# Optimization experiments

Hardware: AMD Instinct MI355X
Metric: run time of the kernel (lower is better)

## Reference

```python
import jax, jax.numpy as jnp
import numpy as np

DT = 0.05
TAU = 10.0
V_TH = 2.0
ALPHA = 1.0 - DT / TAU  # membrane leak factor (1 - dt/tau)


def setup_inputs() -> dict:
    key = jax.random.key(0)
    kx, kw = jax.random.split(key)
    B, T, N = 32, 1024, 2048
    x = jax.random.normal(kx, (B, T, N), dtype=jnp.float32)
    # w ~ Normal(0, 1/sqrt(N)) as in torch.nn.init.normal_(std=1/sqrt(N))
    w = jax.random.normal(kw, (N,), dtype=jnp.float32) * float(1.0 / np.sqrt(N))
    return {"x": x, "w": w}


def reference(x, w):
    """LIF recurrence with online eligibility-trace gradient, fused over time.

    Per step t (matching NeuronClass.__call__ then backward_online):
      v   = alpha*v + x_t @ w - v_th * z          (z from previous step, detached)
      z   = 1[v > v_th]
      eps = x_t - v * w                            # [B, N]
      g  += v * eps + (eps @ w) * p                # p is the PRE-update trace
      p   = alpha*p + x_t
    Returns (v_seq [B,T], z_seq [B,T], grad_acc [B,N]).
    """
    B, T, N = x.shape
    alpha = jnp.asarray(ALPHA, x.dtype)
    v_th = jnp.asarray(V_TH, x.dtype)
    xt = jnp.swapaxes(x, 0, 1)  # [T, B, N] for scan over time

    def step(carry, x_t):
        v, z, p, g = carry
        v = alpha * v + x_t @ w - v_th * z          # [B]
        z = (v > v_th).astype(x_t.dtype)            # hard threshold
        eps = x_t - v[:, None] * w                  # [B, N] prediction error
        g = g + v[:, None] * eps + (eps @ w)[:, None] * p
        p = alpha * p + x_t                         # trace updated AFTER use
        return (v, z, p, g), (v, z)

    v0 = jnp.zeros((B,), x.dtype)
    z0 = jnp.zeros((B,), x.dtype)
    p0 = jnp.zeros((B, N), x.dtype)
    g0 = jnp.zeros((B, N), x.dtype)
    (_, _, _, grad_acc), (v_seq, z_seq) = jax.lax.scan(step, (v0, z0, p0, g0), xt)
    return jnp.swapaxes(v_seq, 0, 1), jnp.swapaxes(z_seq, 0, 1), grad_acc
```

## Files before the change

kernel.cpp:

```cpp
#include <hip/hip_runtime.h>


#define ALPHA 0.995f
#define VTH   2.0f

constexpr int B = 32;
constexpr int T = 1024;
constexpr int N = 2048;
constexpr int CT = 128;
constexpr int NCH = T / CT;
constexpr int TCH = 64;
constexpr int NTC = T / TCH;

__global__ __launch_bounds__(256) void gemv_kernel(const float* __restrict__ x,
                                                   const float* __restrict__ w,
                                                   float* __restrict__ uT) {
    const int wave = threadIdx.x >> 6;
    const int lane = threadIdx.x & 63;
    const int row0 = blockIdx.x * 8 + wave * 2;
    const float* xr0 = x + (size_t)row0 * N;
    const float* xr1 = xr0 + N;
    float s0 = 0.f, s1 = 0.f;
#pragma unroll
    for (int k = 0; k < 8; ++k) {
        const int idx = k * 256 + lane * 4;
        const float4 wv = *reinterpret_cast<const float4*>(w + idx);
        const float4 a  = *reinterpret_cast<const float4*>(xr0 + idx);
        const float4 b  = *reinterpret_cast<const float4*>(xr1 + idx);
        s0 += a.x * wv.x + a.y * wv.y + a.z * wv.z + a.w * wv.w;
        s1 += b.x * wv.x + b.y * wv.y + b.z * wv.z + b.w * wv.w;
    }
#pragma unroll
    for (int off = 32; off; off >>= 1) {
        s0 += __shfl_down(s0, off);
        s1 += __shfl_down(s1, off);
    }
    if (lane == 0) {
        const int b0 = row0 >> 10;
        const int t0 = row0 & 1023;
        uT[t0 * B + b0]       = s0;
        uT[(t0 + 1) * B + b0] = s1;
    }
}

__global__ __launch_bounds__(256) void scan_kernel(const float* __restrict__ w,
                                                   const float* __restrict__ ubuf,
                                                   float* __restrict__ sbuf,
                                                   float* __restrict__ cbuf,
                                                   float* __restrict__ V2,
                                                   float* __restrict__ out_v,
                                                   float* __restrict__ out_z) {
    __shared__ float u_lds[CT * B];
    __shared__ float v_lds[B * (CT + 1)];
    __shared__ float z_lds[B * (CT + 1)];
    __shared__ float red[4];

    const int tid  = threadIdx.x;
    const int wave = tid >> 6;
    const int lane = tid & 63;

    float wacc = 0.f;
#pragma unroll
    for (int i = 0; i < 8; ++i) {
        const float wv = w[i * 256 + tid];
        wacc += wv * wv;
    }
#pragma unroll
    for (int off = 32; off; off >>= 1) wacc += __shfl_xor(wacc, off);
    if (lane == 0) red[wave] = wacc;
    __syncthreads();
    const float wsq = red[0] + red[1] + red[2] + red[3];

    float v = 0.f, z = 0.f, v2 = 0.f;

    for (int cc = 0; cc < NCH; ++cc) {
        const int t0 = cc * CT;
#pragma unroll
        for (int k = 0; k < 4; ++k) {
            const int idx = k * 1024 + tid * 4;
            *reinterpret_cast<float4*>(&u_lds[idx]) =
                *reinterpret_cast<const float4*>(&ubuf[t0 * B + idx]);
        }
        __syncthreads();
        if (tid < 32) {
            const int b = tid;
#pragma unroll 4
            for (int tt = 0; tt < CT; ++tt) {
                const float ut = u_lds[tt * B + b];
                v = ALPHA * v + ut - VTH * z;
                z = (v > VTH) ? 1.f : 0.f;
                v_lds[b * (CT + 1) + tt] = v;
                z_lds[b * (CT + 1) + tt] = z;
                u_lds[tt * B + b] = ut - v * wsq;
                v2 += v * v;
            }
        }
        __syncthreads();
#pragma unroll
        for (int k = 0; k < 4; ++k) {
            const int idx = k * 1024 + tid * 4;
            *reinterpret_cast<float4*>(&sbuf[t0 * B + idx]) =
                *reinterpret_cast<const float4*>(&u_lds[idx]);
        }
#pragma unroll
        for (int k = 0; k < 16; ++k) {
            const int idx = k * 256 + tid;
            const int b  = idx >> 7;
            const int tt = idx & (CT - 1);
            out_v[b * T + t0 + tt] = v_lds[b * (CT + 1) + tt];
            out_z[b * T + t0 + tt] = z_lds[b * (CT + 1) + tt];
        }
        __syncthreads();
    }
    if (tid < 32) V2[tid] = v2;

    float q = 0.f;
    for (int cc = NCH - 1; cc >= 0; --cc) {
        const int t0 = cc * CT;
#pragma unroll
        for (int k = 0; k < 4; ++k) {
            const int idx = k * 1024 + tid * 4;
            *reinterpret_cast<float4*>(&u_lds[idx]) =
                *reinterpret_cast<const float4*>(&sbuf[t0 * B + idx]);
        }
#pragma unroll
        for (int k = 0; k < 16; ++k) {
            const int idx = k * 256 + tid;
            const int b  = idx >> 7;
            const int tt = idx & (CT - 1);
            v_lds[b * (CT + 1) + tt] = out_v[b * T + t0 + tt];
        }
        __syncthreads();
        if (tid < 32) {
            const int b = tid;
#pragma unroll 4
            for (int tt = CT - 1; tt >= 0; --tt) {
                const float st = u_lds[tt * B + b];
                const float vt = v_lds[b * (CT + 1) + tt];
                u_lds[tt * B + b] = vt + q;
                q = st + ALPHA * q;
            }
        }
        __syncthreads();
#pragma unroll
        for (int k = 0; k < 4; ++k) {
            const int idx = k * 1024 + tid * 4;
            *reinterpret_cast<float4*>(&cbuf[t0 * B + idx]) =
                *reinterpret_cast<const float4*>(&u_lds[idx]);
        }
        __syncthreads();
    }
}

__global__ __launch_bounds__(256) void accum_kernel(const float* __restrict__ x,
                                                    const float* __restrict__ cT,
                                                    float* __restrict__ gpart) {
    __shared__ float cs[TCH];
    const int b   = blockIdx.z;
    const int nc  = blockIdx.y;
    const int tc  = blockIdx.x;
    const int t0  = tc * TCH;
    const int tid = threadIdx.x;
    if (tid < TCH) cs[tid] = cT[(t0 + tid) * B + b];
    __syncthreads();

    const int n = nc * 1024 + tid * 4;
    const float* xb = x + ((size_t)b * T + t0) * N + n;
    float4 acc = {0.f, 0.f, 0.f, 0.f};
#pragma unroll 4
    for (int tt = 0; tt < TCH; ++tt) {
        const float4 xv = *reinterpret_cast<const float4*>(xb + (size_t)tt * N);
        const float c = cs[tt];
        acc.x += c * xv.x;
        acc.y += c * xv.y;
        acc.z += c * xv.z;
        acc.w += c * xv.w;
    }
    *reinterpret_cast<float4*>(gpart + ((size_t)tc * B + b) * N + n) = acc;
}

__global__ __launch_bounds__(256) void reduce_kernel(const float* __restrict__ gpart,
                                                     const float* __restrict__ w,
                                                     const float* __restrict__ V2,
                                                     float* __restrict__ g) {
    const int i = blockIdx.x * 256 + threadIdx.x;
    const int b = i >> 11;
    const int n = i & (N - 1);
    float acc = -V2[b] * w[n];
#pragma unroll
    for (int tc = 0; tc < NTC; ++tc) acc += gpart[tc * (B * N) + i];
    g[i] = acc;
}

extern "C" void kernel_launch(void* const* d_in, const int* in_sizes, int n_in,
                              void* d_out, int out_size, void* d_ws, size_t ws_size,
                              hipStream_t stream) {
    const float* x = (const float*)d_in[0];
    const float* w = (const float*)d_in[1];

    float* out   = (float*)d_out;
    float* out_v = out;
    float* out_z = out + B * T;
    float* out_g = out + 2 * B * T;

    float* ubuf  = (float*)d_ws;
    float* sbuf  = ubuf + B * T;
    float* cbuf  = sbuf + B * T;
    float* V2    = cbuf + B * T;
    float* gpart = V2 + B;

    gemv_kernel<<<(B * T) / 8, 256, 0, stream>>>(x, w, ubuf);
    scan_kernel<<<1, 256, 0, stream>>>(w, ubuf, sbuf, cbuf, V2, out_v, out_z);
    accum_kernel<<<dim3(NTC, N / 1024, B), 256, 0, stream>>>(x, cbuf, gpart);
    reduce_kernel<<<(B * N) / 256, 256, 0, stream>>>(gpart, w, V2, out_g);
}
```

Measured before the change: 472.2 us.

## Use nontemporal x loads, wider GEMV rows, larger scan chunks, swizzled LDS

The GEMV now has each wave process four rows instead of two, and the x reads in both GEMV and accum use nontemporal loads to limit cache pollution. The scan chunk grows from 128 to 256 steps and the accum time chunk from 64 to 128. The scan also replaces the padded v/z LDS arrays with one XOR-style swizzled v array and recomputes z from v, and computes wsq per wave without a block sync. The goal is fewer chunk iterations and barriers in the serial scan and better streaming of x, at the cost of fewer accum blocks and more LDS per scan block.

```diff
diff --git a/kernel.cpp b/kernel.cpp
--- a/kernel.cpp
+++ b/kernel.cpp
@@ -7,39 +7,52 @@
 constexpr int B = 32;
 constexpr int T = 1024;
 constexpr int N = 2048;
-constexpr int CT = 128;
+constexpr int CT  = 256;
 constexpr int NCH = T / CT;
-constexpr int TCH = 64;
+constexpr int TCH = 128;
 constexpr int NTC = T / TCH;
+
+typedef float floatx4 __attribute__((ext_vector_type(4)));
+
+__device__ inline floatx4 ntload4(const float* p) {
+    return __builtin_nontemporal_load(reinterpret_cast<const floatx4*>(p));
+}
 
 __global__ __launch_bounds__(256) void gemv_kernel(const float* __restrict__ x,
                                                    const float* __restrict__ w,
                                                    float* __restrict__ uT) {
     const int wave = threadIdx.x >> 6;
     const int lane = threadIdx.x & 63;
-    const int row0 = blockIdx.x * 8 + wave * 2;
-    const float* xr0 = x + (size_t)row0 * N;
-    const float* xr1 = xr0 + N;
-    float s0 = 0.f, s1 = 0.f;
+    const int row0 = blockIdx.x * 16 + wave * 4;
+    const float* xr = x + (size_t)row0 * N;
+    float s0 = 0.f, s1 = 0.f, s2 = 0.f, s3 = 0.f;
 #pragma unroll
     for (int k = 0; k < 8; ++k) {
         const int idx = k * 256 + lane * 4;
-        const float4 wv = *reinterpret_cast<const float4*>(w + idx);
-        const float4 a  = *reinterpret_cast<const float4*>(xr0 + idx);
-        const float4 b  = *reinterpret_cast<const float4*>(xr1 + idx);
+        const floatx4 wv = *reinterpret_cast<const floatx4*>(w + idx);
+        const floatx4 a = ntload4(xr + idx);
+        const floatx4 b = ntload4(xr + N + idx);
+        const floatx4 c = ntload4(xr + 2 * N + idx);
+        const floatx4 d = ntload4(xr + 3 * N + idx);
         s0 += a.x * wv.x + a.y * wv.y + a.z * wv.z + a.w * wv.w;
         s1 += b.x * wv.x + b.y * wv.y + b.z * wv.z + b.w * wv.w;
+        s2 += c.x * wv.x + c.y * wv.y + c.z * wv.z + c.w * wv.w;
+        s3 += d.x * wv.x + d.y * wv.y + d.z * wv.z + d.w * wv.w;
     }
 #pragma unroll
     for (int off = 32; off; off >>= 1) {
         s0 += __shfl_down(s0, off);
         s1 += __shfl_down(s1, off);
+        s2 += __shfl_down(s2, off);
+        s3 += __shfl_down(s3, off);
     }
     if (lane == 0) {
         const int b0 = row0 >> 10;
         const int t0 = row0 & 1023;
-        uT[t0 * B + b0]       = s0;
+        uT[(t0 + 0) * B + b0] = s0;
         uT[(t0 + 1) * B + b0] = s1;
+        uT[(t0 + 2) * B + b0] = s2;
+        uT[(t0 + 3) * B + b0] = s3;
     }
 }
 
@@ -51,64 +64,59 @@
                                                    float* __restrict__ out_v,
                                                    float* __restrict__ out_z) {
     __shared__ float u_lds[CT * B];
-    __shared__ float v_lds[B * (CT + 1)];
-    __shared__ float z_lds[B * (CT + 1)];
-    __shared__ float red[4];
-
+    __shared__ float v_st[CT * B];
     const int tid  = threadIdx.x;
-    const int wave = tid >> 6;
     const int lane = tid & 63;
 
     float wacc = 0.f;
 #pragma unroll
-    for (int i = 0; i < 8; ++i) {
-        const float wv = w[i * 256 + tid];
+    for (int i = 0; i < N / 64; ++i) {
+        const float wv = w[i * 64 + lane];
         wacc += wv * wv;
     }
 #pragma unroll
     for (int off = 32; off; off >>= 1) wacc += __shfl_xor(wacc, off);
-    if (lane == 0) red[wave] = wacc;
-    __syncthreads();
-    const float wsq = red[0] + red[1] + red[2] + red[3];
+    const float wsq = wacc;
 
     float v = 0.f, z = 0.f, v2 = 0.f;
 
     for (int cc = 0; cc < NCH; ++cc) {
-        const int t0 = cc * CT;
-#pragma unroll
-        for (int k = 0; k < 4; ++k) {
-            const int idx = k * 1024 + tid * 4;
-            *reinterpret_cast<float4*>(&u_lds[idx]) =
-                *reinterpret_cast<const float4*>(&ubuf[t0 * B + idx]);
+        const int base = cc * CT * B;
+        const int t0   = cc * CT;
+#pragma unroll
+        for (int k = 0; k < 8; ++k) {
+            const int j = k * 1024 + tid * 4;
+            *reinterpret_cast<floatx4*>(&u_lds[j]) =
+                *reinterpret_cast<const floatx4*>(&ubuf[base + j]);
         }
         __syncthreads();
         if (tid < 32) {
             const int b = tid;
 #pragma unroll 4
             for (int tt = 0; tt < CT; ++tt) {
-                const float ut = u_lds[tt * B + b];
+                const float ut = u_lds[tt * 32 + b];
                 v = ALPHA * v + ut - VTH * z;
                 z = (v > VTH) ? 1.f : 0.f;
-                v_lds[b * (CT + 1) + tt] = v;
-                z_lds[b * (CT + 1) + tt] = z;
-                u_lds[tt * B + b] = ut - v * wsq;
+                u_lds[tt * 32 + b] = ut - v * wsq;
+                v_st[tt * 32 + ((b + tt) & 31)] = v;
                 v2 += v * v;
             }
         }
         __syncthreads();
 #pragma unroll
-        for (int k = 0; k < 4; ++k) {
-            const int idx = k * 1024 + tid * 4;
-            *reinterpret_cast<float4*>(&sbuf[t0 * B + idx]) =
-                *reinterpret_cast<const float4*>(&u_lds[idx]);
-        }
-#pragma unroll
-        for (int k = 0; k < 16; ++k) {
+        for (int k = 0; k < 8; ++k) {
+            const int j = k * 1024 + tid * 4;
+            *reinterpret_cast<floatx4*>(&sbuf[base + j]) =
+                *reinterpret_cast<const floatx4*>(&u_lds[j]);
+        }
+#pragma unroll
+        for (int k = 0; k < 32; ++k) {
             const int idx = k * 256 + tid;
-            const int b  = idx >> 7;
-            const int tt = idx & (CT - 1);
-            out_v[b * T + t0 + tt] = v_lds[b * (CT + 1) + tt];
-            out_z[b * T + t0 + tt] = z_lds[b * (CT + 1) + tt];
+            const int b  = idx >> 8;
+            const int tt = idx & 255;
+            const float vv = v_st[tt * 32 + ((b + tt) & 31)];
+            out_v[b * T + t0 + tt] = vv;
+            out_z[b * T + t0 + tt] = (vv > VTH) ? 1.f : 0.f;
         }
         __syncthreads();
     }
@@ -116,37 +124,38 @@
 
     float q = 0.f;
     for (int cc = NCH - 1; cc >= 0; --cc) {
-        const int t0 = cc * CT;
-#pragma unroll
-        for (int k = 0; k < 4; ++k) {
-            const int idx = k * 1024 + tid * 4;
-            *reinterpret_cast<float4*>(&u_lds[idx]) =
-                *reinterpret_cast<const float4*>(&sbuf[t0 * B + idx]);
-        }
-#pragma unroll
-        for (int k = 0; k < 16; ++k) {
+        const int base = cc * CT * B;
+        const int t0   = cc * CT;
+#pragma unroll
+        for (int k = 0; k < 8; ++k) {
+            const int j = k * 1024 + tid * 4;
+            *reinterpret_cast<floatx4*>(&u_lds[j]) =
+                *reinterpret_cast<const floatx4*>(&sbuf[base + j]);
+        }
+#pragma unroll
+        for (int k = 0; k < 32; ++k) {
             const int idx = k * 256 + tid;
-            const int b  = idx >> 7;
-            const int tt = idx & (CT - 1);
-            v_lds[b * (CT + 1) + tt] = out_v[b * T + t0 + tt];
+            const int b  = idx >> 8;
+            const int tt = idx & 255;
+            v_st[tt * 32 + ((b + tt) & 31)] = out_v[b * T + t0 + tt];
         }
         __syncthreads();
         if (tid < 32) {
             const int b = tid;
 #pragma unroll 4
             for (int tt = CT - 1; tt >= 0; --tt) {
-                const float st = u_lds[tt * B + b];
-                const float vt = v_lds[b * (CT + 1) + tt];
-                u_lds[tt * B + b] = vt + q;
+                const float st = u_lds[tt * 32 + b];
+                const float vt = v_st[tt * 32 + ((b + tt) & 31)];
+                u_lds[tt * 32 + b] = vt + q;
                 q = st + ALPHA * q;
             }
         }
         __syncthreads();
 #pragma unroll
-        for (int k = 0; k < 4; ++k) {
-            const int idx = k * 1024 + tid * 4;
-            *reinterpret_cast<float4*>(&cbuf[t0 * B + idx]) =
-                *reinterpret_cast<const float4*>(&u_lds[idx]);
+        for (int k = 0; k < 8; ++k) {
+            const int j = k * 1024 + tid * 4;
+            *reinterpret_cast<floatx4*>(&cbuf[base + j]) =
+                *reinterpret_cast<const floatx4*>(&u_lds[j]);
         }
         __syncthreads();
     }
@@ -166,17 +175,17 @@
 
     const int n = nc * 1024 + tid * 4;
     const float* xb = x + ((size_t)b * T + t0) * N + n;
-    float4 acc = {0.f, 0.f, 0.f, 0.f};
+    floatx4 acc = {0.f, 0.f, 0.f, 0.f};
 #pragma unroll 4
     for (int tt = 0; tt < TCH; ++tt) {
-        const float4 xv = *reinterpret_cast<const float4*>(xb + (size_t)tt * N);
+        const floatx4 xv = ntload4(xb + (size_t)tt * N);
         const float c = cs[tt];
         acc.x += c * xv.x;
         acc.y += c * xv.y;
         acc.z += c * xv.z;
         acc.w += c * xv.w;
     }
-    *reinterpret_cast<float4*>(gpart + ((size_t)tc * B + b) * N + n) = acc;
+    *reinterpret_cast<floatx4*>(gpart + ((size_t)tc * B + b) * N + n) = acc;
 }
 
 __global__ __launch_bounds__(256) void reduce_kernel(const float* __restrict__ gpart,
@@ -209,7 +218,7 @@
     float* V2    = cbuf + B * T;
     float* gpart = V2 + B;
 
-    gemv_kernel<<<(B * T) / 8, 256, 0, stream>>>(x, w, ubuf);
+    gemv_kernel<<<(B * T) / 16, 256, 0, stream>>>(x, w, ubuf);
     scan_kernel<<<1, 256, 0, stream>>>(w, ubuf, sbuf, cbuf, V2, out_v, out_z);
     accum_kernel<<<dim3(NTC, N / 1024, B), 256, 0, stream>>>(x, cbuf, gpart);
     reduce_kernel<<<(B * N) / 256, 256, 0, stream>>>(gpart, w, V2, out_g);
```

Result: faster. 461.9 us (-2.2%).
